# Optimization experiments

Hardware: AMD Instinct MI355X
Metric: run time of the kernel (lower is better)

## Reference

```python
import jax, jax.numpy as jnp
import numpy as np

B = 8
N_GENES = 19836
D_IN = 11
D_H = 64
DEG = 16
N = B * N_GENES
E_PER = N_GENES * DEG


def setup_inputs() -> dict:
    key = jax.random.key(0)
    ks = jax.random.split(key, 20)
    x = jax.random.normal(ks[0], (B, N_GENES, D_IN), dtype=jnp.float32)
    # edges: random within each graph, offset by graph index
    base_src = jax.random.randint(ks[1], (B, E_PER), 0, N_GENES)
    base_dst = jax.random.randint(ks[2], (B, E_PER), 0, N_GENES)
    offs = (jnp.arange(B) * N_GENES)[:, None]
    src = (base_src + offs).reshape(-1).astype(jnp.int64) if False else (base_src + offs).reshape(-1)
    dst = (base_dst + offs).reshape(-1)
    s = 0.02
    def nrm(k, shape):
        return jax.random.normal(k, shape, dtype=jnp.float32) * s
    return {
        'x': x, 'src': src, 'dst': dst,
        'enc_W': nrm(ks[3], (D_H, D_IN)), 'enc_b': jnp.zeros((D_H,), jnp.float32),
        'gene_emb': nrm(ks[4], (N_GENES, D_H)),
        'gin_W': nrm(ks[5], (D_H, D_H)),
        'bn_w': 1.0 + nrm(ks[6], (D_H,)), 'bn_b': jnp.zeros((D_H,), jnp.float32),
        'key_W': nrm(ks[7], (D_H, D_H)), 'key_b': jnp.zeros((D_H,), jnp.float32),
        'query_w': nrm(ks[8], (1, D_H)),
        'val_W': nrm(ks[9], (D_H, D_H)), 'val_b': jnp.zeros((D_H,), jnp.float32),
        'sae_enc_W': nrm(ks[10], (D_H, D_H)), 'sae_enc_b': jnp.zeros((D_H,), jnp.float32),
        'sae_dec_W': nrm(ks[11], (D_H, D_H)), 'sae_dec_b': jnp.zeros((D_H,), jnp.float32),
        'pred_W1': nrm(ks[12], (D_H, D_H)), 'pred_b1': jnp.zeros((D_H,), jnp.float32),
        'pred_W2': nrm(ks[13], (1, D_H)), 'pred_b2': jnp.zeros((1,), jnp.float32),
    }


def gelu(x):
    return jax.nn.gelu(x, approximate=False)  # nn.GELU default = exact erf


def batchnorm(h, w, b, eps=1e-5):
    # training-mode BatchNorm1d: batch statistics, biased variance
    mu = jnp.mean(h, axis=0)
    var = jnp.mean((h - mu) ** 2, axis=0)
    return (h - mu) * jax.lax.rsqrt(var + eps) * w + b


def reference(x, src, dst, enc_W, enc_b, gene_emb, gin_W, bn_w, bn_b,
              key_W, key_b, query_w, val_W, val_b,
              sae_enc_W, sae_enc_b, sae_dec_W, sae_dec_b,
              pred_W1, pred_b1, pred_W2, pred_b2):
    bsz, n_gene, d_in = x.shape
    n_nodes = bsz * n_gene
    # gene encoder: single Linear (bias) + GELU (inner batchnorm result is discarded in source)
    h = gelu(x.reshape(-1, d_in) @ enc_W.T + enc_b)          # [N, D_H]
    h = (h.reshape(bsz, n_gene, -1) + gene_emb).reshape(n_nodes, -1)
    # GIN layer (eps=0, sum aggregation): MLP(h + sum_{u->v} h_u); MLP = single Linear, no bias
    agg = jax.ops.segment_sum(h[src], dst, num_segments=n_nodes)  # irregular gather/scatter
    h = (h + agg) @ gin_W.T
    h = gelu(batchnorm(h, bn_w, bn_b))
    # attentive readout with SAE
    keys = h @ key_W.T + key_b
    w = jax.nn.sigmoid(keys @ query_w.T)                     # [N, 1]
    v = h @ val_W.T + val_b
    z = v * w
    enc = jax.nn.relu(z @ sae_enc_W.T + sae_enc_b)
    dec = enc @ sae_dec_W.T + sae_dec_b
    sae_loss = jnp.mean((dec - z) ** 2) + 1.0 * jnp.mean(jnp.abs(enc))
    gid = jnp.arange(n_nodes) // n_gene
    g_h = jax.ops.segment_sum(dec * w, gid, num_segments=bsz)  # [B, D_H]
    # predictor: Linear+GELU, Linear (inner batchnorm discarded in source)
    preds = gelu(g_h @ pred_W1.T + pred_b1) @ pred_W2.T + pred_b2
    return preds, w, sae_loss, dec
```

## Files before the change

### kernel.cpp

```cpp
#include <hip/hip_runtime.h>
#include <hip/hip_bf16.h>
#include <math.h>

#define NGENES 19836
#define BATCH 8
#define DIN 11
#define DH 64
#define NNODES (BATCH * NGENES)
#define E_PER (NGENES * 16)
#define NEDGES (NNODES * 16)
#define NDH (NNODES * DH)
#define NWAVE ((NNODES + 63) / 64)
#define NBLK_POST ((NWAVE + 3) / 4)
#define TPAD 65

#define SCAN_CHUNK 1024
#define NSBLK ((NNODES + SCAN_CHUNK - 1) / SCAN_CHUNK)

#define OUT_PREDS 0
#define OUT_W 8
#define OUT_SAE (8 + NNODES)
#define OUT_DEC (9 + NNODES)

__device__ __forceinline__ float gelu_f(float x) {
    return 0.5f * x * (1.0f + erff(x * 0.70710678118654752f));
}

__device__ __forceinline__ float bcast(float v, int lane) {
    return __int_as_float(__builtin_amdgcn_readlane(__float_as_int(v), lane));
}

__device__ __forceinline__ float wave_sum(float v) {
    #pragma unroll
    for (int o = 32; o; o >>= 1) v += __shfl_xor(v, o, 64);
    return v;
}

__global__ void k_encoder(const float* __restrict__ x, const float* __restrict__ encW,
                          const float* __restrict__ encB, const float* __restrict__ gemb,
                          __hip_bfloat16* __restrict__ h16) {
    int lane = threadIdx.x & 63;
    int g = blockIdx.x & 7;
    int wix = (blockIdx.x >> 3) * (blockDim.x >> 6) + (threadIdx.x >> 6);
    int wper = (gridDim.x >> 3) * (blockDim.x >> 6);
    float wreg[DIN];
    #pragma unroll
    for (int k = 0; k < DIN; ++k) wreg[k] = encW[lane * DIN + k];
    float bias = encB[lane];
    size_t gb = (size_t)g * NGENES;
    for (int i = wix; i < NGENES; i += wper) {
        size_t node = gb + i;
        const float* xr = x + node * DIN;
        float acc = bias;
        #pragma unroll
        for (int k = 0; k < DIN; ++k) acc = fmaf(xr[k], wreg[k], acc);
        float hv = gelu_f(acc) + gemb[(size_t)i * DH + lane];
        h16[node * DH + lane] = __float2bfloat16(hv);
    }
}

__global__ void k_hist(const int* __restrict__ dst, int* __restrict__ counts) {
    int g = blockIdx.x & 7;
    int t = (blockIdx.x >> 3) * blockDim.x + threadIdx.x;
    int nt = (gridDim.x >> 3) * blockDim.x;
    const int* dg = dst + (size_t)g * E_PER;
    for (int e = t; e < E_PER; e += nt)
        atomicAdd(&counts[dg[e]], 1);
}

__global__ void k_scan1(const int* __restrict__ counts, int* __restrict__ bsum) {
    __shared__ int red[256];
    int base = blockIdx.x * SCAN_CHUNK + threadIdx.x * 4;
    int s = 0;
    #pragma unroll
    for (int i = 0; i < 4; ++i) {
        int n = base + i;
        if (n < NNODES) s += counts[n];
    }
    red[threadIdx.x] = s;
    __syncthreads();
    for (int o = 128; o; o >>= 1) {
        if (threadIdx.x < o) red[threadIdx.x] += red[threadIdx.x + o];
        __syncthreads();
    }
    if (threadIdx.x == 0) bsum[blockIdx.x] = red[0];
}

__global__ void k_scan2(const int* __restrict__ bsum, int* __restrict__ boff) {
    __shared__ int red[256];
    int t = threadIdx.x;
    int v = (t < NSBLK) ? bsum[t] : 0;
    red[t] = v;
    __syncthreads();
    for (int o = 1; o < 256; o <<= 1) {
        int u = (t >= o) ? red[t - o] : 0;
        __syncthreads();
        red[t] += u;
        __syncthreads();
    }
    if (t < NSBLK) boff[t] = red[t] - v;
}

__global__ void k_scan3(const int* __restrict__ counts, const int* __restrict__ boff,
                        int* __restrict__ offsets, int* __restrict__ cursor) {
    __shared__ int red[256];
    int t = threadIdx.x;
    int base = blockIdx.x * SCAN_CHUNK + t * 4;
    int c[4];
    int s = 0;
    #pragma unroll
    for (int i = 0; i < 4; ++i) {
        int n = base + i;
        c[i] = (n < NNODES) ? counts[n] : 0;
        s += c[i];
    }
    red[t] = s;
    __syncthreads();
    for (int o = 1; o < 256; o <<= 1) {
        int v = (t >= o) ? red[t - o] : 0;
        __syncthreads();
        red[t] += v;
        __syncthreads();
    }
    int excl = red[t] - s + boff[blockIdx.x];
    #pragma unroll
    for (int i = 0; i < 4; ++i) {
        int n = base + i;
        if (n < NNODES) { offsets[n] = excl; cursor[n] = excl; }
        excl += c[i];
    }
}

__global__ void k_scatter(const int* __restrict__ src, const int* __restrict__ dst,
                          int* __restrict__ cursor, unsigned short* __restrict__ csr) {
    int g = blockIdx.x & 7;
    int t = (blockIdx.x >> 3) * blockDim.x + threadIdx.x;
    int nt = (gridDim.x >> 3) * blockDim.x;
    const int* sg = src + (size_t)g * E_PER;
    const int* dg = dst + (size_t)g * E_PER;
    int gbase = g * NGENES;
    for (int e = t; e < E_PER; e += nt) {
        int p = atomicAdd(&cursor[dg[e]], 1);
        csr[p] = (unsigned short)(sg[e] - gbase);
    }
}

__global__ void __launch_bounds__(256, 4)
k_aggin(const __hip_bfloat16* __restrict__ h16, const int* __restrict__ offsets,
        const int* __restrict__ counts, const unsigned short* __restrict__ csr,
        const float* __restrict__ ginW, float* __restrict__ h2,
        float* __restrict__ stats) {
    __shared__ float ldsW[DH * DH];
    __shared__ float red[2][256];
    for (int idx = threadIdx.x; idx < DH * DH; idx += 256) {
        int k = idx >> 6, d = idx & 63;
        ldsW[idx] = ginW[d * DH + k];
    }
    __syncthreads();
    int lane = threadIdx.x & 63;
    int g = blockIdx.x & 7;
    int wix = (blockIdx.x >> 3) * 4 + (threadIdx.x >> 6);
    int wper = (gridDim.x >> 3) * 4;
    int gbase = g * NGENES;
    float s1 = 0.f, s2 = 0.f;
    for (int i = wix; i < NGENES; i += wper) {
        int node = gbase + i;
        float a[8];
        a[0] = __bfloat162float(h16[(size_t)node * DH + lane]);
        #pragma unroll
        for (int u = 1; u < 8; ++u) a[u] = 0.f;
        int start = offsets[node];
        int cnt = counts[node];
        for (int e0 = 0; e0 < cnt; e0 += 64) {
            int nn = min(64, cnt - e0);
            int iv = (lane < nn) ? (int)csr[start + e0 + lane] : 0;
            int j = 0;
            for (; j + 7 < nn; j += 8) {
                #pragma unroll
                for (int u = 0; u < 8; ++u) {
                    int v = gbase + __shfl(iv, j + u, 64);
                    a[u] += __bfloat162float(h16[(size_t)v * DH + lane]);
                }
            }
            for (; j < nn; ++j)
                a[0] += __bfloat162float(h16[(size_t)(gbase + __shfl(iv, j, 64)) * DH + lane]);
        }
        float tval = ((a[0] + a[1]) + (a[2] + a[3])) + ((a[4] + a[5]) + (a[6] + a[7]));
        float m0 = 0.f, m1 = 0.f, m2 = 0.f, m3 = 0.f;
        #pragma unroll
        for (int k = 0; k < DH; k += 4) {
            m0 = fmaf(ldsW[(k + 0) * DH + lane], bcast(tval, k + 0), m0);
            m1 = fmaf(ldsW[(k + 1) * DH + lane], bcast(tval, k + 1), m1);
            m2 = fmaf(ldsW[(k + 2) * DH + lane], bcast(tval, k + 2), m2);
            m3 = fmaf(ldsW[(k + 3) * DH + lane], bcast(tval, k + 3), m3);
        }
        float outv = (m0 + m1) + (m2 + m3);
        h2[(size_t)node * DH + lane] = outv;
        s1 += outv;
        s2 += outv * outv;
    }
    red[0][threadIdx.x] = s1;
    red[1][threadIdx.x] = s2;
    __syncthreads();
    if (threadIdx.x < 64) {
        float t1 = red[0][threadIdx.x] + red[0][threadIdx.x + 64] + red[0][threadIdx.x + 128] + red[0][threadIdx.x + 192];
        float t2 = red[1][threadIdx.x] + red[1][threadIdx.x + 64] + red[1][threadIdx.x + 128] + red[1][threadIdx.x + 192];
        atomicAdd(&stats[threadIdx.x], t1);
        atomicAdd(&stats[64 + threadIdx.x], t2);
    }
}

__global__ void k_bnparams(const float* __restrict__ stats, const float* __restrict__ bnw,
                           const float* __restrict__ bnb, const float* __restrict__ keyW,
                           const float* __restrict__ keyB, const float* __restrict__ qw,
                           float* __restrict__ bnp) {
    int d = threadIdx.x;
    float inv_n = 1.0f / (float)NNODES;
    float mu = stats[d] * inv_n;
    float var = stats[64 + d] * inv_n - mu * mu;
    float sc = bnw[d] * rsqrtf(var + 1e-5f);
    bnp[d] = sc;
    bnp[64 + d] = bnb[d] - mu * sc;
    float kq0 = 0.f, kq1 = 0.f;
    #pragma unroll
    for (int j = 0; j < DH; j += 2) {
        kq0 = fmaf(qw[j], keyW[j * DH + d], kq0);
        kq1 = fmaf(qw[j + 1], keyW[(j + 1) * DH + d], kq1);
    }
    bnp[128 + d] = kq0 + kq1;
    float qb = wave_sum(qw[d] * keyB[d]);
    if (d == 0) bnp[192] = qb;
}

__global__ void __launch_bounds__(256, 2)
k_post(const float* __restrict__ h2, const float* __restrict__ bnp,
       const float* __restrict__ valW, const float* __restrict__ valB,
       const float* __restrict__ encW, const float* __restrict__ encB,
       const float* __restrict__ decW, const float* __restrict__ decB,
       float* __restrict__ decout, float* __restrict__ wout,
       float* __restrict__ g_h, float* __restrict__ loss) {
    __shared__ float tile[4][64 * TPAD];
    __shared__ float wqs[4][64];
    int lane = threadIdx.x & 63;
    int w = threadIdx.x >> 6;
    int wg = blockIdx.x * 4 + w;
    int tn = wg * 64;
    if (tn >= NNODES) return;
    float* T = tile[w];

    {
        const float* srcp = h2 + (size_t)tn * DH;
        #pragma unroll
        for (int j = 0; j < 16; ++j) {
            int fid = j * 64 + lane;
            int r = fid >> 4, c = (fid & 15) * 4;
            float4 v = make_float4(0.f, 0.f, 0.f, 0.f);
            if (tn + r < NNODES)
                v = *reinterpret_cast<const float4*>(srcp + (size_t)fid * 4);
            float* d = T + r * TPAD + c;
            d[0] = v.x; d[1] = v.y; d[2] = v.z; d[3] = v.w;
        }
    }
    __builtin_amdgcn_wave_barrier();

    int node = tn + lane;
    bool act = node < NNODES;
    float* row = T + lane * TPAD;
    float v64[DH];

    float p = bnp[192];
    #pragma unroll
    for (int k = 0; k < DH; ++k) {
        float hv = gelu_f(fmaf(row[k], bnp[k], bnp[64 + k]));
        v64[k] = hv;
        p = fmaf(hv, bnp[128 + k], p);
    }
    float wq = 1.0f / (1.0f + expf(-p));
    if (act) wout[node] = wq;
    wqs[w][lane] = act ? wq : 0.f;

    #pragma unroll 1
    for (int d4 = 0; d4 < DH; d4 += 4) {
        float a0 = valB[d4], a1 = valB[d4 + 1], a2 = valB[d4 + 2], a3 = valB[d4 + 3];
        #pragma unroll
        for (int k = 0; k < DH; ++k) {
            float hk = v64[k];
            a0 = fmaf(valW[(d4 + 0) * DH + k], hk, a0);
            a1 = fmaf(valW[(d4 + 1) * DH + k], hk, a1);
            a2 = fmaf(valW[(d4 + 2) * DH + k], hk, a2);
            a3 = fmaf(valW[(d4 + 3) * DH + k], hk, a3);
        }
        row[d4 + 0] = a0 * wq; row[d4 + 1] = a1 * wq;
        row[d4 + 2] = a2 * wq; row[d4 + 3] = a3 * wq;
    }

    float l1 = 0.f;
    #pragma unroll 1
    for (int d4 = 0; d4 < DH; d4 += 4) {
        float a0 = encB[d4], a1 = encB[d4 + 1], a2 = encB[d4 + 2], a3 = encB[d4 + 3];
        #pragma unroll
        for (int k = 0; k < DH; ++k) {
            float zk = row[k];
            a0 = fmaf(encW[(d4 + 0) * DH + k], zk, a0);
            a1 = fmaf(encW[(d4 + 1) * DH + k], zk, a1);
            a2 = fmaf(encW[(d4 + 2) * DH + k], zk, a2);
            a3 = fmaf(encW[(d4 + 3) * DH + k], zk, a3);
        }
        a0 = fmaxf(a0, 0.f); a1 = fmaxf(a1, 0.f);
        a2 = fmaxf(a2, 0.f); a3 = fmaxf(a3, 0.f);
        l1 += (a0 + a1) + (a2 + a3);
        v64[d4 + 0] = a0; v64[d4 + 1] = a1; v64[d4 + 2] = a2; v64[d4 + 3] = a3;
    }

    float sq = 0.f;
    #pragma unroll 1
    for (int d4 = 0; d4 < DH; d4 += 4) {
        float a0 = decB[d4], a1 = decB[d4 + 1], a2 = decB[d4 + 2], a3 = decB[d4 + 3];
        #pragma unroll
        for (int k = 0; k < DH; ++k) {
            float ek = v64[k];
            a0 = fmaf(decW[(d4 + 0) * DH + k], ek, a0);
            a1 = fmaf(decW[(d4 + 1) * DH + k], ek, a1);
            a2 = fmaf(decW[(d4 + 2) * DH + k], ek, a2);
            a3 = fmaf(decW[(d4 + 3) * DH + k], ek, a3);
        }
        float z0 = row[d4 + 0], z1 = row[d4 + 1], z2 = row[d4 + 2], z3 = row[d4 + 3];
        float e0 = a0 - z0, e1 = a1 - z1, e2 = a2 - z2, e3 = a3 - z3;
        sq += (e0 * e0 + e1 * e1) + (e2 * e2 + e3 * e3);
        row[d4 + 0] = a0; row[d4 + 1] = a1; row[d4 + 2] = a2; row[d4 + 3] = a3;
    }
    __builtin_amdgcn_wave_barrier();

    {
        float* dstp = decout + (size_t)tn * DH;
        #pragma unroll
        for (int j = 0; j < 16; ++j) {
            int fid = j * 64 + lane;
            int r = fid >> 4, c = (fid & 15) * 4;
            if (tn + r < NNODES) {
                const float* s = T + r * TPAD + c;
                float4 v = { s[0], s[1], s[2], s[3] };
                *reinterpret_cast<float4*>(dstp + (size_t)fid * 4) = v;
            }
        }
    }

    {
        int g0 = tn / NGENES;
        int bnd = (g0 + 1) * NGENES - tn;
        if (bnd > 64) bnd = 64;
        float acc0 = 0.f, acc1 = 0.f;
        for (int r = 0; r < 64; ++r) {
            float v = T[r * TPAD + lane] * wqs[w][r];
            if (r < bnd) acc0 += v; else acc1 += v;
        }
        atomicAdd(&g_h[g0 * DH + lane], acc0);
        if (bnd < 64 && g0 + 1 < BATCH)
            atomicAdd(&g_h[(g0 + 1) * DH + lane], acc1);
    }

    if (!act) { l1 = 0.f; sq = 0.f; }
    sq = wave_sum(sq);
    l1 = wave_sum(l1);
    if (lane == 0) {
        atomicAdd(&loss[0], sq);
        atomicAdd(&loss[1], l1);
    }
}

__global__ void k_pred(const float* __restrict__ g_h, const float* __restrict__ W1,
                       const float* __restrict__ b1, const float* __restrict__ W2,
                       const float* __restrict__ b2, const float* __restrict__ loss,
                       float* __restrict__ out) {
    int lane = threadIdx.x;
    float w1[DH];
    #pragma unroll
    for (int k = 0; k < DH; ++k) w1[k] = W1[lane * DH + k];
    float bb = b1[lane], w2 = W2[lane];
    for (int g = 0; g < BATCH; ++g) {
        float gh = g_h[g * DH + lane];
        float a0 = 0.f, a1 = 0.f;
        #pragma unroll
        for (int k = 0; k < DH; k += 2) {
            a0 = fmaf(w1[k], bcast(gh, k), a0);
            a1 = fmaf(w1[k + 1], bcast(gh, k + 1), a1);
        }
        float t = gelu_f(a0 + a1 + bb);
        float p = wave_sum(t * w2);
        if (lane == 0) out[OUT_PREDS + g] = p + b2[0];
    }
    if (lane == 0) out[OUT_SAE] = (loss[0] + loss[1]) * (1.0f / ((float)NNODES * (float)DH));
}

extern "C" void kernel_launch(void* const* d_in, const int* in_sizes, int n_in,
                              void* d_out, int out_size, void* d_ws, size_t ws_size,
                              hipStream_t stream) {
    const float* x    = (const float*)d_in[0];
    const int* src    = (const int*)d_in[1];
    const int* dst    = (const int*)d_in[2];
    const float* encW = (const float*)d_in[3];
    const float* encB = (const float*)d_in[4];
    const float* gemb = (const float*)d_in[5];
    const float* ginW = (const float*)d_in[6];
    const float* bnw  = (const float*)d_in[7];
    const float* bnb  = (const float*)d_in[8];
    const float* keyW = (const float*)d_in[9];
    const float* keyB = (const float*)d_in[10];
    const float* qw   = (const float*)d_in[11];
    const float* valW = (const float*)d_in[12];
    const float* valB = (const float*)d_in[13];
    const float* saeEncW = (const float*)d_in[14];
    const float* saeEncB = (const float*)d_in[15];
    const float* saeDecW = (const float*)d_in[16];
    const float* saeDecB = (const float*)d_in[17];
    const float* pW1  = (const float*)d_in[18];
    const float* pb1  = (const float*)d_in[19];
    const float* pW2  = (const float*)d_in[20];
    const float* pb2  = (const float*)d_in[21];

    float* out = (float*)d_out;
    float* ws = (float*)d_ws;

    int*   counts  = (int*)ws;
    float* stats   = ws + NNODES;
    float* g_h     = stats + 128;
    float* loss    = g_h + 512;
    float* bnp     = loss + 2;
    int*   offsets = (int*)(bnp + 256);
    int*   cursor  = offsets + NNODES;
    unsigned short* csr = (unsigned short*)(cursor + NNODES);
    int*   bsum    = (int*)(csr + NEDGES);
    int*   boff    = bsum + 256;
    float* h2      = (float*)(boff + 256);

    __hip_bfloat16* h16 = (__hip_bfloat16*)(out + OUT_DEC);
    float* decregion = out + OUT_DEC;
    float* wout = out + OUT_W;

    hipMemsetAsync(d_ws, 0, (size_t)(NNODES + 642) * sizeof(float), stream);

    k_encoder<<<2048, 256, 0, stream>>>(x, encW, encB, gemb, h16);
    k_hist<<<2048, 256, 0, stream>>>(dst, counts);
    k_scan1<<<NSBLK, 256, 0, stream>>>(counts, bsum);
    k_scan2<<<1, 256, 0, stream>>>(bsum, boff);
    k_scan3<<<NSBLK, 256, 0, stream>>>(counts, boff, offsets, cursor);
    k_scatter<<<2048, 256, 0, stream>>>(src, dst, cursor, csr);
    k_aggin<<<2048, 256, 0, stream>>>(h16, offsets, counts, csr, ginW, h2, stats);
    k_bnparams<<<1, 64, 0, stream>>>(stats, bnw, bnb, keyW, keyB, qw, bnp);
    k_post<<<NBLK_POST, 256, 0, stream>>>(h2, bnp, valW, valB,
                                          saeEncW, saeEncB, saeDecW, saeDecB,
                                          decregion, wout, g_h, loss);
    k_pred<<<1, 64, 0, stream>>>(g_h, pW1, pb1, pW2, pb2, loss, out);
}
```

Before: 828.1 us.

## Fold SAE encoder into value projection and split post kernel into two stages

Precomputes M1 = encW·valW and encW·valB in a tiny kernel, so the SAE encoder input is computed directly from h as wq·(M1·h + encW·valB) + encB instead of materialising z first. The post stage is split into k_postA, which applies BN+GELU, computes the attention weight and writes h3 transposed in bf16, and k_postB, which runs the fused encoder, decoder and value GEMVs with weights pre-transposed for broadcast loads. The aim is to cut the serial dependency chain and keep 64-wide accumulator arrays in registers. In exchange it adds an extra global round-trip through h3t, recomputes the value projection for the loss, and stores intermediates in bf16, which changes precision.

```diff
diff --git a/kernel.cpp b/kernel.cpp
--- a/kernel.cpp
+++ b/kernel.cpp
@@ -10,9 +10,6 @@
 #define E_PER (NGENES * 16)
 #define NEDGES (NNODES * 16)
 #define NDH (NNODES * DH)
-#define NWAVE ((NNODES + 63) / 64)
-#define NBLK_POST ((NWAVE + 3) / 4)
-#define TPAD 65
 
 #define SCAN_CHUNK 1024
 #define NSBLK ((NNODES + SCAN_CHUNK - 1) / SCAN_CHUNK)
@@ -56,6 +53,29 @@
         for (int k = 0; k < DIN; ++k) acc = fmaf(xr[k], wreg[k], acc);
         float hv = gelu_f(acc) + gemb[(size_t)i * DH + lane];
         h16[node * DH + lane] = __float2bfloat16(hv);
+    }
+}
+
+__global__ void k_prew(const float* __restrict__ encW, const float* __restrict__ valW,
+                       const float* __restrict__ valB, const float* __restrict__ decW,
+                       float* __restrict__ M1t, float* __restrict__ m1v,
+                       float* __restrict__ valWT, float* __restrict__ decWT) {
+    int tid = threadIdx.x;
+    for (int e = tid; e < DH * DH; e += 256) {
+        int d = e >> 6, k = e & 63;
+        float acc = 0.f;
+        #pragma unroll 4
+        for (int j = 0; j < DH; ++j)
+            acc = fmaf(encW[d * DH + j], valW[j * DH + k], acc);
+        M1t[k * DH + d] = acc;
+        valWT[k * DH + d] = valW[d * DH + k];
+        decWT[k * DH + d] = decW[d * DH + k];
+    }
+    if (tid < DH) {
+        float acc = 0.f;
+        for (int j = 0; j < DH; ++j)
+            acc = fmaf(encW[tid * DH + j], valB[j], acc);
+        m1v[tid] = acc;
     }
 }
 
@@ -232,102 +252,103 @@
     if (d == 0) bnp[192] = qb;
 }
 
-__global__ void __launch_bounds__(256, 2)
-k_post(const float* __restrict__ h2, const float* __restrict__ bnp,
-       const float* __restrict__ valW, const float* __restrict__ valB,
-       const float* __restrict__ encW, const float* __restrict__ encB,
-       const float* __restrict__ decW, const float* __restrict__ decB,
-       float* __restrict__ decout, float* __restrict__ wout,
-       float* __restrict__ g_h, float* __restrict__ loss) {
-    __shared__ float tile[4][64 * TPAD];
-    __shared__ float wqs[4][64];
+__global__ void __launch_bounds__(256, 4)
+k_postA(const float* __restrict__ h2, const float* __restrict__ bnp,
+        __hip_bfloat16* __restrict__ h3t, float* __restrict__ wout) {
+    int node = blockIdx.x * 256 + threadIdx.x;
+    bool act = node < NNODES;
+    int nc = act ? node : 0;
+    const float* srcp = h2 + (size_t)nc * DH;
+    float h3[DH];
+    #pragma unroll
+    for (int j = 0; j < 16; ++j) {
+        float4 v = *reinterpret_cast<const float4*>(srcp + j * 4);
+        h3[j * 4 + 0] = v.x; h3[j * 4 + 1] = v.y;
+        h3[j * 4 + 2] = v.z; h3[j * 4 + 3] = v.w;
+    }
+    float p = bnp[192];
+    #pragma unroll
+    for (int k = 0; k < DH; ++k) {
+        float hv = gelu_f(fmaf(h3[k], bnp[k], bnp[64 + k]));
+        h3[k] = hv;
+        p = fmaf(hv, bnp[128 + k], p);
+    }
+    float wq = 1.0f / (1.0f + expf(-p));
+    if (act) {
+        wout[node] = wq;
+        #pragma unroll
+        for (int k = 0; k < DH; ++k)
+            h3t[(size_t)k * NNODES + node] = __float2bfloat16(h3[k]);
+    }
+}
+
+__global__ void __launch_bounds__(128, 4)
+k_postB(const __hip_bfloat16* __restrict__ h3t, const float* __restrict__ wout,
+        const float* __restrict__ M1t, const float* __restrict__ m1v,
+        const float* __restrict__ encB, const float* __restrict__ decWT,
+        const float* __restrict__ decB, const float* __restrict__ valWT,
+        const float* __restrict__ valB, float* __restrict__ decout,
+        float* __restrict__ g_h, float* __restrict__ loss) {
+    __shared__ float tile[2][DH * 66];
+    __shared__ float wqs[2][64];
     int lane = threadIdx.x & 63;
     int w = threadIdx.x >> 6;
-    int wg = blockIdx.x * 4 + w;
-    int tn = wg * 64;
-    if (tn >= NNODES) return;
-    float* T = tile[w];
-
-    {
-        const float* srcp = h2 + (size_t)tn * DH;
-        #pragma unroll
-        for (int j = 0; j < 16; ++j) {
-            int fid = j * 64 + lane;
-            int r = fid >> 4, c = (fid & 15) * 4;
-            float4 v = make_float4(0.f, 0.f, 0.f, 0.f);
-            if (tn + r < NNODES)
-                v = *reinterpret_cast<const float4*>(srcp + (size_t)fid * 4);
-            float* d = T + r * TPAD + c;
-            d[0] = v.x; d[1] = v.y; d[2] = v.z; d[3] = v.w;
-        }
-    }
-    __builtin_amdgcn_wave_barrier();
-
+    int tn = (blockIdx.x * 2 + w) * 64;
     int node = tn + lane;
     bool act = node < NNODES;
-    float* row = T + lane * TPAD;
-    float v64[DH];
-
-    float p = bnp[192];
-    #pragma unroll
+    int nc = act ? node : 0;
+    float* T = tile[w];
+    __hip_bfloat16* E = (__hip_bfloat16*)T;
+
+    float wq = act ? wout[node] : 0.f;
+    wqs[w][lane] = wq;
+
+    float acc[DH];
+
+    #pragma unroll
+    for (int d = 0; d < DH; ++d) acc[d] = 0.f;
+    #pragma unroll 1
     for (int k = 0; k < DH; ++k) {
-        float hv = gelu_f(fmaf(row[k], bnp[k], bnp[64 + k]));
-        v64[k] = hv;
-        p = fmaf(hv, bnp[128 + k], p);
-    }
-    float wq = 1.0f / (1.0f + expf(-p));
-    if (act) wout[node] = wq;
-    wqs[w][lane] = act ? wq : 0.f;
-
+        float h3k = __bfloat162float(h3t[(size_t)k * NNODES + nc]);
+        #pragma unroll
+        for (int d = 0; d < DH; ++d)
+            acc[d] = fmaf(M1t[k * DH + d], h3k, acc[d]);
+    }
+    float l1 = 0.f;
+    #pragma unroll
+    for (int d = 0; d < DH; ++d) {
+        float e = fmaxf(fmaf(wq, acc[d] + m1v[d], encB[d]), 0.f);
+        l1 += e;
+        E[lane * 66 + d] = __float2bfloat16(e);
+    }
+
+    #pragma unroll
+    for (int d = 0; d < DH; ++d) acc[d] = decB[d];
     #pragma unroll 1
-    for (int d4 = 0; d4 < DH; d4 += 4) {
-        float a0 = valB[d4], a1 = valB[d4 + 1], a2 = valB[d4 + 2], a3 = valB[d4 + 3];
-        #pragma unroll
-        for (int k = 0; k < DH; ++k) {
-            float hk = v64[k];
-            a0 = fmaf(valW[(d4 + 0) * DH + k], hk, a0);
-            a1 = fmaf(valW[(d4 + 1) * DH + k], hk, a1);
-            a2 = fmaf(valW[(d4 + 2) * DH + k], hk, a2);
-            a3 = fmaf(valW[(d4 + 3) * DH + k], hk, a3);
-        }
-        row[d4 + 0] = a0 * wq; row[d4 + 1] = a1 * wq;
-        row[d4 + 2] = a2 * wq; row[d4 + 3] = a3 * wq;
-    }
-
-    float l1 = 0.f;
+    for (int k = 0; k < DH; ++k) {
+        float ek = __bfloat162float(E[lane * 66 + k]);
+        #pragma unroll
+        for (int d = 0; d < DH; ++d)
+            acc[d] = fmaf(decWT[k * DH + d], ek, acc[d]);
+    }
+    #pragma unroll
+    for (int d = 0; d < DH; ++d) T[lane * 66 + d] = acc[d];
+
+    #pragma unroll
+    for (int d = 0; d < DH; ++d) acc[d] = 0.f;
     #pragma unroll 1
-    for (int d4 = 0; d4 < DH; d4 += 4) {
-        float a0 = encB[d4], a1 = encB[d4 + 1], a2 = encB[d4 + 2], a3 = encB[d4 + 3];
-        #pragma unroll
-        for (int k = 0; k < DH; ++k) {
-            float zk = row[k];
-            a0 = fmaf(encW[(d4 + 0) * DH + k], zk, a0);
-            a1 = fmaf(encW[(d4 + 1) * DH + k], zk, a1);
-            a2 = fmaf(encW[(d4 + 2) * DH + k], zk, a2);
-            a3 = fmaf(encW[(d4 + 3) * DH + k], zk, a3);
-        }
-        a0 = fmaxf(a0, 0.f); a1 = fmaxf(a1, 0.f);
-        a2 = fmaxf(a2, 0.f); a3 = fmaxf(a3, 0.f);
-        l1 += (a0 + a1) + (a2 + a3);
-        v64[d4 + 0] = a0; v64[d4 + 1] = a1; v64[d4 + 2] = a2; v64[d4 + 3] = a3;
-    }
-
+    for (int k = 0; k < DH; ++k) {
+        float h3k = __bfloat162float(h3t[(size_t)k * NNODES + nc]);
+        #pragma unroll
+        for (int d = 0; d < DH; ++d)
+            acc[d] = fmaf(valWT[k * DH + d], h3k, acc[d]);
+    }
     float sq = 0.f;
-    #pragma unroll 1
-    for (int d4 = 0; d4 < DH; d4 += 4) {
-        float a0 = decB[d4], a1 = decB[d4 + 1], a2 = decB[d4 + 2], a3 = decB[d4 + 3];
-        #pragma unroll
-        for (int k = 0; k < DH; ++k) {
-            float ek = v64[k];
-            a0 = fmaf(decW[(d4 + 0) * DH + k], ek, a0);
-            a1 = fmaf(decW[(d4 + 1) * DH + k], ek, a1);
-            a2 = fmaf(decW[(d4 + 2) * DH + k], ek, a2);
-            a3 = fmaf(decW[(d4 + 3) * DH + k], ek, a3);
-        }
-        float z0 = row[d4 + 0], z1 = row[d4 + 1], z2 = row[d4 + 2], z3 = row[d4 + 3];
-        float e0 = a0 - z0, e1 = a1 - z1, e2 = a2 - z2, e3 = a3 - z3;
-        sq += (e0 * e0 + e1 * e1) + (e2 * e2 + e3 * e3);
-        row[d4 + 0] = a0; row[d4 + 1] = a1; row[d4 + 2] = a2; row[d4 + 3] = a3;
+    #pragma unroll
+    for (int d = 0; d < DH; ++d) {
+        float z = wq * (acc[d] + valB[d]);
+        float df = T[lane * 66 + d] - z;
+        sq = fmaf(df, df, sq);
     }
     __builtin_amdgcn_wave_barrier();
 
@@ -338,7 +359,7 @@
             int fid = j * 64 + lane;
             int r = fid >> 4, c = (fid & 15) * 4;
             if (tn + r < NNODES) {
-                const float* s = T + r * TPAD + c;
+                const float* s = T + r * 66 + c;
                 float4 v = { s[0], s[1], s[2], s[3] };
                 *reinterpret_cast<float4*>(dstp + (size_t)fid * 4) = v;
             }
@@ -351,7 +372,7 @@
         if (bnd > 64) bnd = 64;
         float acc0 = 0.f, acc1 = 0.f;
         for (int r = 0; r < 64; ++r) {
-            float v = T[r * TPAD + lane] * wqs[w][r];
+            float v = T[r * 66 + lane] * wqs[w][r];
             if (r < bnd) acc0 += v; else acc1 += v;
         }
         atomicAdd(&g_h[g0 * DH + lane], acc0);
@@ -359,7 +380,7 @@
             atomicAdd(&g_h[(g0 + 1) * DH + lane], acc1);
     }
 
-    if (!act) { l1 = 0.f; sq = 0.f; }
+    if (!act) { sq = 0.f; l1 = 0.f; }
     sq = wave_sum(sq);
     l1 = wave_sum(l1);
     if (lane == 0) {
@@ -425,20 +446,26 @@
     float* stats   = ws + NNODES;
     float* g_h     = stats + 128;
     float* loss    = g_h + 512;
-    float* bnp     = loss + 2;
-    int*   offsets = (int*)(bnp + 256);
+    float* bnp     = loss + 4;
+    float* M1t     = bnp + 256;
+    float* m1v     = M1t + 4096;
+    float* valWT   = m1v + 64;
+    float* decWT   = valWT + 4096;
+    int*   offsets = (int*)(decWT + 4096);
     int*   cursor  = offsets + NNODES;
     unsigned short* csr = (unsigned short*)(cursor + NNODES);
     int*   bsum    = (int*)(csr + NEDGES);
     int*   boff    = bsum + 256;
     float* h2      = (float*)(boff + 256);
+    __hip_bfloat16* h3t = (__hip_bfloat16*)(h2 + NDH);
 
     __hip_bfloat16* h16 = (__hip_bfloat16*)(out + OUT_DEC);
     float* decregion = out + OUT_DEC;
     float* wout = out + OUT_W;
 
-    hipMemsetAsync(d_ws, 0, (size_t)(NNODES + 642) * sizeof(float), stream);
-
+    hipMemsetAsync(d_ws, 0, (size_t)(NNODES + 648) * sizeof(float), stream);
+
+    k_prew<<<1, 256, 0, stream>>>(saeEncW, valW, valB, saeDecW, M1t, m1v, valWT, decWT);
     k_encoder<<<2048, 256, 0, stream>>>(x, encW, encB, gemb, h16);
     k_hist<<<2048, 256, 0, stream>>>(dst, counts);
     k_scan1<<<NSBLK, 256, 0, stream>>>(counts, bsum);
@@ -447,8 +474,9 @@
     k_scatter<<<2048, 256, 0, stream>>>(src, dst, cursor, csr);
     k_aggin<<<2048, 256, 0, stream>>>(h16, offsets, counts, csr, ginW, h2, stats);
     k_bnparams<<<1, 64, 0, stream>>>(stats, bnw, bnb, keyW, keyB, qw, bnp);
-    k_post<<<NBLK_POST, 256, 0, stream>>>(h2, bnp, valW, valB,
-                                          saeEncW, saeEncB, saeDecW, saeDecB,
-                                          decregion, wout, g_h, loss);
+    k_postA<<<(NNODES + 255) / 256, 256, 0, stream>>>(h2, bnp, h3t, wout);
+    k_postB<<<(NNODES + 127) / 128, 128, 0, stream>>>(h3t, wout, M1t, m1v, saeEncB,
+                                                      decWT, saeDecB, valWT, valB,
+                                                      decregion, g_h, loss);
     k_pred<<<1, 64, 0, stream>>>(g_h, pW1, pb1, pW2, pb2, loss, out);
 }
```

New measurement: 803.3 us. 1.03x faster.
